# Optimization experiments

Measured on AMD Instinct MI355X. Metric: run time of the kernel, lower is better.

The kernel has to match this reference:

```python
import jax, jax.numpy as jnp
import numpy as np

NUM_HEADS = 16
Q_HEAD_DIM = 128
KV_HEAD_DIM = 128
ROPE_DIM = 64
LATENT_DIM = 512
INPUT_DIM = 2048


def setup_inputs() -> dict:
    key = jax.random.key(0)
    ks = jax.random.split(key, 7)
    B, S, D = 2, 2048, INPUT_DIM
    x = jax.random.normal(ks[0], (B, S, D), dtype=jnp.float32)
    positions = jnp.arange(S, dtype=jnp.int32)
    # weights stored as (in, out); torch Linear computes x @ W.T with W:(out,in)
    sc = lambda fan_in: 1.0 / np.sqrt(fan_in)
    Wq = jax.random.normal(ks[1], (D, NUM_HEADS * Q_HEAD_DIM), dtype=jnp.float32) * sc(D)
    Wc = jax.random.normal(ks[2], (D, LATENT_DIM), dtype=jnp.float32) * sc(D)
    Wk = jax.random.normal(ks[3], (LATENT_DIM, NUM_HEADS * KV_HEAD_DIM), dtype=jnp.float32) * sc(LATENT_DIM)
    Wv = jax.random.normal(ks[4], (LATENT_DIM, NUM_HEADS * KV_HEAD_DIM), dtype=jnp.float32) * sc(LATENT_DIM)
    Wo = jax.random.normal(ks[5], (NUM_HEADS * KV_HEAD_DIM, D), dtype=jnp.float32) * sc(NUM_HEADS * KV_HEAD_DIM)
    return {"x": x, "positions": positions, "Wq": Wq, "Wc": Wc, "Wk": Wk, "Wv": Wv, "Wo": Wo}


def _apply_rope_q(q, positions):
    # partial RoPE on first ROPE_DIM dims of q: (B,S,H,Dq)
    half = ROPE_DIM // 2
    inv_freq = 1.0 / (10000.0 ** (jnp.arange(0, ROPE_DIM, 2, dtype=jnp.float32) / ROPE_DIM))
    freqs = positions.astype(jnp.float32)[:, None] * inv_freq[None, :]  # (S, half)
    cos = jnp.cos(freqs)[None, :, None, :]  # (1,S,1,half)
    sin = jnp.sin(freqs)[None, :, None, :]
    x1 = q[..., :half]
    x2 = q[..., half:ROPE_DIM]
    rotated = jnp.concatenate([x1 * cos - x2 * sin, x1 * sin + x2 * cos], axis=-1)
    return jnp.concatenate([rotated, q[..., ROPE_DIM:]], axis=-1)


def reference(x, positions, Wq, Wc, Wk, Wv, Wo):
    B, S, _ = x.shape
    H, Dq, Dk = NUM_HEADS, Q_HEAD_DIM, KV_HEAD_DIM
    q = (x @ Wq).reshape(B, S, H, Dq)
    kv_latent = x @ Wc                       # (B,S,latent) low-rank compression
    k = (kv_latent @ Wk).reshape(B, S, H, Dk)
    v = (kv_latent @ Wv).reshape(B, S, H, Dk)
    q = _apply_rope_q(q, positions)          # RoPE applied to q only (as in source)
    scale = 1.0 / jnp.sqrt(jnp.float32(Dq))
    scores = jnp.einsum("bqhd,bkhd->bhqk", q, k) * scale
    attn = jax.nn.softmax(scores, axis=-1)
    out = jnp.einsum("bhqk,bkhd->bqhd", attn, v).reshape(B, S, H * Dk)
    return out @ Wo
```

## Files before the change

kernel.cpp:

```cpp
#include <hip/hip_runtime.h>
#include <math.h>


typedef __attribute__((ext_vector_type(8))) short bf16x8;
typedef __attribute__((ext_vector_type(4))) float f32x4;
typedef __attribute__((ext_vector_type(16))) float f32x16;

#define GLDS(gp, lp)                                                         \
  __builtin_amdgcn_global_load_lds(                                          \
      (const __attribute__((address_space(1))) void*)(gp),                   \
      (__attribute__((address_space(3))) void*)(lp), 16, 0, 0)

__device__ __forceinline__ short f2bf(float f) {
  unsigned u = __builtin_bit_cast(unsigned, f);
  u += 0x7fffu + ((u >> 16) & 1u);
  return (short)(u >> 16);
}
__device__ __forceinline__ float b2f(short x) {
  unsigned u = ((unsigned)(unsigned short)x) << 16;
  return __builtin_bit_cast(float, u);
}
__device__ __forceinline__ unsigned cvtpk(float lo, float hi) {
  unsigned r;
  asm("v_cvt_pk_bf16_f32 %0, %1, %2" : "=v"(r) : "v"(lo), "v"(hi));
  return r;
}

__global__ void cast4_kernel(const float* __restrict__ x, short* __restrict__ xb, int n4) {
  int i = blockIdx.x * blockDim.x + threadIdx.x;
  if (i < n4) {
    float4 v = ((const float4*)x)[i];
    ushort4 o;
    o.x = (unsigned short)f2bf(v.x);
    o.y = (unsigned short)f2bf(v.y);
    o.z = (unsigned short)f2bf(v.z);
    o.w = (unsigned short)f2bf(v.w);
    ((ushort4*)xb)[i] = o;
  }
}

__global__ void transpose_cast_kernel(const float* __restrict__ W, short* __restrict__ Wt,
                                      int K, int N) {
  __shared__ float tile[32][33];
  int n0 = blockIdx.x * 32, k0 = blockIdx.y * 32;
  int tx = threadIdx.x & 31, ty = threadIdx.x >> 5;
#pragma unroll
  for (int i = 0; i < 4; ++i)
    tile[ty + i * 8][tx] = W[(size_t)(k0 + ty + i * 8) * N + n0 + tx];
  __syncthreads();
#pragma unroll
  for (int i = 0; i < 4; ++i)
    Wt[(size_t)(n0 + ty + i * 8) * K + k0 + tx] = f2bf(tile[tx][ty + i * 8]);
}

__global__ void rope_tab_kernel(const int* __restrict__ pos, float* __restrict__ cosT,
                                float* __restrict__ sinT) {
  int idx = blockIdx.x * 256 + threadIdx.x;
  if (idx < 2048 * 32) {
    int s = idx >> 5, i = idx & 31;
    float p = (float)pos[s];
    float freq = p * powf(10000.0f, -(float)(2 * i) / 64.0f);
    float sv, cv;
    sincosf(freq, &sv, &cv);
    cosT[idx] = cv;
    sinT[idx] = sv;
  }
}

template <int MODE>
__global__ __launch_bounds__(256, 2) void gemm_bt(const short* __restrict__ A,
                                                  const short* __restrict__ Bt,
                                                  void* __restrict__ Cv,
                                                  int M, int N, int K) {
  __shared__ alignas(16) short sm[16384];
  const int tid  = threadIdx.x;
  const int lane = tid & 63;
  const int w    = tid >> 6;
  const int col  = lane & 15, g = lane >> 4;
  const int bm = blockIdx.y * 128, bn = blockIdx.x * 128;
  const int wr = w >> 1, wc = w & 1;

  f32x4 zero4 = {0.f, 0.f, 0.f, 0.f};
  f32x4 acc[4][4];
#pragma unroll
  for (int m = 0; m < 4; ++m)
#pragma unroll
    for (int n = 0; n < 4; ++n) acc[m][n] = zero4;

  const int srow = tid >> 2;
  const int skel = (tid & 3) * 8;
  const short* ag = A + (size_t)(bm + srow) * K + skel;
  const short* bg = Bt + (size_t)(bn + srow) * K + skel;

  auto STAGE = [&](int buf, int t) {
#pragma unroll
    for (int i = 0; i < 2; ++i) {
      GLDS(ag + (size_t)t * 32 + (size_t)i * 64 * K, sm + buf * 4096 + i * 2048 + w * 512);
      GLDS(bg + (size_t)t * 32 + (size_t)i * 64 * K, sm + 8192 + buf * 4096 + i * 2048 + w * 512);
    }
  };

  const int nt = K >> 5;
  STAGE(0, 0);
  __syncthreads();
  int buf = 0;
  for (int t = 0; t < nt; ++t) {
    if (t + 1 < nt) STAGE(buf ^ 1, t + 1);
    const short* As = sm + buf * 4096;
    const short* Bs = sm + 8192 + buf * 4096;
    bf16x8 la[4], lb[4];
#pragma unroll
    for (int m = 0; m < 4; ++m)
      la[m] = *(const bf16x8*)(As + (wr * 64 + m * 16 + col) * 32 + g * 8);
#pragma unroll
    for (int n = 0; n < 4; ++n)
      lb[n] = *(const bf16x8*)(Bs + (wc * 64 + n * 16 + col) * 32 + g * 8);
#pragma unroll
    for (int m = 0; m < 4; ++m)
#pragma unroll
      for (int n = 0; n < 4; ++n)
        acc[m][n] = __builtin_amdgcn_mfma_f32_16x16x32_bf16(la[m], lb[n], acc[m][n], 0, 0, 0);
    __syncthreads();
    buf ^= 1;
  }

  const int orow0 = bm + wr * 64;
  const int ocol0 = bn + wc * 64;
  if (MODE == 0) {
    short* C = (short*)Cv;
#pragma unroll
    for (int m = 0; m < 4; ++m)
#pragma unroll
      for (int n = 0; n < 4; ++n)
#pragma unroll
        for (int r = 0; r < 4; ++r)
          C[(size_t)(orow0 + m * 16 + g * 4 + r) * N + ocol0 + n * 16 + col] =
              f2bf(acc[m][n][r]);
  } else if (MODE == 1) {
    float* C = (float*)Cv;
#pragma unroll
    for (int m = 0; m < 4; ++m)
#pragma unroll
      for (int n = 0; n < 4; ++n)
#pragma unroll
        for (int r = 0; r < 4; ++r)
          C[(size_t)(orow0 + m * 16 + g * 4 + r) * N + ocol0 + n * 16 + col] =
              acc[m][n][r];
  } else {
    short* C = (short*)Cv;
#pragma unroll
    for (int m = 0; m < 4; ++m)
#pragma unroll
      for (int n = 0; n < 4; ++n) {
        int grow = orow0 + m * 16 + g * 4;
        int bb = grow >> 11, s = grow & 2047;
        int cn = ocol0 + n * 16 + col;
        ushort4 pk;
        pk.x = (unsigned short)f2bf(acc[m][n][0]);
        pk.y = (unsigned short)f2bf(acc[m][n][1]);
        pk.z = (unsigned short)f2bf(acc[m][n][2]);
        pk.w = (unsigned short)f2bf(acc[m][n][3]);
        *(ushort4*)(C + ((size_t)(bb * 2048 + cn)) * 2048 + s) = pk;
      }
  }
}

__global__ __launch_bounds__(256, 2) void attn_kernel(
    const short* __restrict__ qb, const short* __restrict__ kb,
    const short* __restrict__ vt, short* __restrict__ ob,
    const float* __restrict__ cosT, const float* __restrict__ sinT) {
  __shared__ alignas(16) short sm[32768];
  const int lane = threadIdx.x & 63, w = threadIdx.x >> 6;
  const int ql = lane & 31, hi = lane >> 5;
  const int qt = blockIdx.x >> 5, bh = blockIdx.x & 31;
  const int b = bh >> 4, h = bh & 15;
  const int q0w = qt * 128 + w * 32;
  const int qrow = q0w + ql;

  bf16x8 qf[8];
  {
    const short* qp = qb + ((size_t)(b * 2048 + qrow)) * 2048 + h * 128;
#pragma unroll
    for (int db = 0; db < 8; ++db) qf[db] = *(const bf16x8*)(qp + db * 16 + hi * 8);
    const float* cp = cosT + qrow * 32;
    const float* sp = sinT + qrow * 32;
#pragma unroll
    for (int db = 0; db < 2; ++db)
#pragma unroll
      for (int j = 0; j < 8; ++j) {
        int i = db * 16 + hi * 8 + j;
        float x1 = b2f(qf[db][j]), x2 = b2f(qf[db + 2][j]);
        float cv = cp[i], sv = sp[i];
        qf[db][j]     = f2bf(x1 * cv - x2 * sv);
        qf[db + 2][j] = f2bf(x1 * sv + x2 * cv);
      }
  }

  f32x16 o[4];
#pragma unroll
  for (int m4 = 0; m4 < 4; ++m4)
#pragma unroll
    for (int r = 0; r < 16; ++r) o[m4][r] = 0.f;
  float mrun = -3.0e38f, lrun = 0.f;

  auto STAGE = [&](int buf, int kt) {
#pragma unroll
    for (int i = 0; i < 4; ++i) {
      int r = w * 16 + i * 4 + (lane >> 4);
      int cch = lane & 15;
      const short* gp = kb + ((size_t)(b * 2048 + kt * 64 + r)) * 2048 + h * 128 +
                        ((cch ^ (r & 7)) << 3);
      GLDS(gp, sm + buf * 8192 + w * 2048 + i * 512);
    }
#pragma unroll
    for (int i = 0; i < 4; ++i) {
      int rd = w * 32 + i * 8 + (lane >> 3);
      int cch = lane & 7;
      const short* gp = vt + ((size_t)(b * 2048 + h * 128 + rd)) * 2048 + kt * 64 +
                        ((cch ^ (rd & 7)) << 3);
      GLDS(gp, sm + 16384 + buf * 8192 + w * 2048 + i * 512);
    }
  };

  const float cl2 = 0.12752744590518352f;
  STAGE(0, 0);
  __syncthreads();
  int buf = 0;
  for (int kt = 0; kt < 32; ++kt) {
    if (kt + 1 < 32) STAGE(buf ^ 1, kt + 1);
    const short* Ks = sm + buf * 8192;
    const short* Vs = sm + 16384 + buf * 8192;

    f32x16 skt[2];
    __builtin_amdgcn_s_setprio(1);
#pragma unroll
    for (int kb2 = 0; kb2 < 2; ++kb2) {
      f32x16 a;
#pragma unroll
      for (int r = 0; r < 16; ++r) a[r] = 0.f;
      int krow = kb2 * 32 + ql;
#pragma unroll
      for (int db = 0; db < 8; ++db) {
        bf16x8 kf = *(const bf16x8*)(Ks + krow * 128 + (((db * 2 + hi) ^ (krow & 7)) << 3));
        a = __builtin_amdgcn_mfma_f32_32x32x16_bf16(kf, qf[db], a, 0, 0, 0);
      }
      skt[kb2] = a;
    }
    __builtin_amdgcn_s_setprio(0);

#pragma unroll
    for (int kb2 = 0; kb2 < 2; ++kb2)
#pragma unroll
      for (int r = 0; r < 16; ++r) skt[kb2][r] *= cl2;

    float t0, t1, t2, t3;
    t0 = fmaxf(fmaxf(fmaxf(fmaxf(skt[0][0], skt[0][4]), skt[0][8]),
                     fmaxf(skt[0][12], skt[1][0])),
               fmaxf(fmaxf(skt[1][4], skt[1][8]), skt[1][12]));
    t1 = fmaxf(fmaxf(fmaxf(fmaxf(skt[0][1], skt[0][5]), skt[0][9]),
                     fmaxf(skt[0][13], skt[1][1])),
               fmaxf(fmaxf(skt[1][5], skt[1][9]), skt[1][13]));
    t2 = fmaxf(fmaxf(fmaxf(fmaxf(skt[0][2], skt[0][6]), skt[0][10]),
                     fmaxf(skt[0][14], skt[1][2])),
               fmaxf(fmaxf(skt[1][6], skt[1][10]), skt[1][14]));
    t3 = fmaxf(fmaxf(fmaxf(fmaxf(skt[0][3], skt[0][7]), skt[0][11]),
                     fmaxf(skt[0][15], skt[1][3])),
               fmaxf(fmaxf(skt[1][7], skt[1][11]), skt[1][15]));
    float tmax = fmaxf(fmaxf(t0, t1), fmaxf(t2, t3));
    tmax = fmaxf(tmax, __shfl_xor(tmax, 32));

    if (!__all(tmax <= mrun + 8.0f)) {
      float mn = fmaxf(mrun, tmax);
      float fr = __builtin_amdgcn_exp2f(mrun - mn);
      mrun = mn;
      lrun *= fr;
#pragma unroll
      for (int m4 = 0; m4 < 4; ++m4)
#pragma unroll
        for (int r = 0; r < 16; ++r) o[m4][r] *= fr;
    }
    float s0 = 0.f, s1 = 0.f, s2 = 0.f, s3 = 0.f;
#pragma unroll
    for (int kb2 = 0; kb2 < 2; ++kb2)
#pragma unroll
      for (int r = 0; r < 16; r += 4) {
        skt[kb2][r]     = __builtin_amdgcn_exp2f(skt[kb2][r] - mrun);
        skt[kb2][r + 1] = __builtin_amdgcn_exp2f(skt[kb2][r + 1] - mrun);
        skt[kb2][r + 2] = __builtin_amdgcn_exp2f(skt[kb2][r + 2] - mrun);
        skt[kb2][r + 3] = __builtin_amdgcn_exp2f(skt[kb2][r + 3] - mrun);
        s0 += skt[kb2][r];     s1 += skt[kb2][r + 1];
        s2 += skt[kb2][r + 2]; s3 += skt[kb2][r + 3];
      }
    float psum = (s0 + s1) + (s2 + s3);
    psum += __shfl_xor(psum, 32);
    lrun += psum;

    bf16x8 pf[4];
#pragma unroll
    for (int kb2 = 0; kb2 < 2; ++kb2) {
#pragma unroll
      for (int half = 0; half < 2; ++half) {
        unsigned a0 = cvtpk(skt[kb2][half * 8 + 0], skt[kb2][half * 8 + 1]);
        unsigned a1 = cvtpk(skt[kb2][half * 8 + 2], skt[kb2][half * 8 + 3]);
        unsigned b0 = cvtpk(skt[kb2][half * 8 + 4], skt[kb2][half * 8 + 5]);
        unsigned b1 = cvtpk(skt[kb2][half * 8 + 6], skt[kb2][half * 8 + 7]);
        unsigned pa0 = __shfl_xor(a0, 32), pa1 = __shfl_xor(a1, 32);
        unsigned pb0 = __shfl_xor(b0, 32), pb1 = __shfl_xor(b1, 32);
        union { unsigned u[4]; bf16x8 v; } tmp;
        tmp.u[0] = hi ? pb0 : a0;
        tmp.u[1] = hi ? pb1 : a1;
        tmp.u[2] = hi ? b0 : pa0;
        tmp.u[3] = hi ? b1 : pa1;
        pf[kb2 * 2 + half] = tmp.v;
      }
    }

    __builtin_amdgcn_s_setprio(1);
#pragma unroll
    for (int m4 = 0; m4 < 4; ++m4) {
      int rd = m4 * 32 + ql;
#pragma unroll
      for (int ks = 0; ks < 4; ++ks) {
        bf16x8 vf = *(const bf16x8*)(Vs + rd * 64 + (((ks * 2 + hi) ^ (rd & 7)) << 3));
        o[m4] = __builtin_amdgcn_mfma_f32_32x32x16_bf16(vf, pf[ks], o[m4], 0, 0, 0);
      }
    }
    __builtin_amdgcn_s_setprio(0);
    __syncthreads();
    buf ^= 1;
  }

  float il = 1.0f / lrun;
  short* E = sm + w * 4352;
#pragma unroll
  for (int m4 = 0; m4 < 4; ++m4)
#pragma unroll
    for (int r = 0; r < 16; r += 2) {
      int d = m4 * 32 + (r & 3) + 8 * (r >> 2) + 4 * hi;
      unsigned pk = cvtpk(o[m4][r] * il, o[m4][r + 1] * il);
      *(unsigned*)(E + ql * 136 + d) = pk;
    }
  asm volatile("s_waitcnt lgkmcnt(0)" ::: "memory");
#pragma unroll
  for (int it = 0; it < 8; ++it) {
    int row = it * 4 + (lane >> 4);
    int ch = lane & 15;
    bf16x8 v = *(const bf16x8*)(E + row * 136 + ch * 8);
    *(bf16x8*)(ob + ((size_t)(b * 2048 + q0w + row)) * 2048 + h * 128 + ch * 8) = v;
  }
}

extern "C" void kernel_launch(void* const* d_in, const int* in_sizes, int n_in,
                              void* d_out, int out_size, void* d_ws, size_t ws_size,
                              hipStream_t stream) {
  (void)in_sizes; (void)n_in; (void)out_size; (void)ws_size;
  const float* x  = (const float*)d_in[0];
  const int*   pos = (const int*)d_in[1];
  const float* Wq = (const float*)d_in[2];
  const float* Wc = (const float*)d_in[3];
  const float* Wk = (const float*)d_in[4];
  const float* Wv = (const float*)d_in[5];
  const float* Wo = (const float*)d_in[6];

  char* ws = (char*)d_ws;
  short* xb   = (short*)(ws);
  short* qb   = (short*)(ws + 16777216);
  short* kvb  = (short*)(ws + 33554432);
  short* kb   = (short*)(ws + 37748736);
  short* vtb  = (short*)(ws + 54525952);
  short* obuf = (short*)(ws + 71303168);
  short* wqT  = (short*)(ws + 88080384);
  short* wcT  = (short*)(ws + 96468992);
  short* wkT  = (short*)(ws + 98566144);
  short* wvT  = (short*)(ws + 100663296);
  short* woT  = (short*)(ws + 102760448);
  float* cosT = (float*)(ws + 111149056);
  float* sinT = (float*)(ws + 111411200);

  cast4_kernel<<<8192, 256, 0, stream>>>(x, xb, 2097152);
  transpose_cast_kernel<<<dim3(64, 64), 256, 0, stream>>>(Wq, wqT, 2048, 2048);
  transpose_cast_kernel<<<dim3(16, 64), 256, 0, stream>>>(Wc, wcT, 2048, 512);
  transpose_cast_kernel<<<dim3(64, 16), 256, 0, stream>>>(Wk, wkT, 512, 2048);
  transpose_cast_kernel<<<dim3(64, 16), 256, 0, stream>>>(Wv, wvT, 512, 2048);
  transpose_cast_kernel<<<dim3(64, 64), 256, 0, stream>>>(Wo, woT, 2048, 2048);
  rope_tab_kernel<<<256, 256, 0, stream>>>(pos, cosT, sinT);

  gemm_bt<0><<<dim3(16, 32), 256, 0, stream>>>(xb, wqT, qb, 4096, 2048, 2048);
  gemm_bt<0><<<dim3(4, 32), 256, 0, stream>>>(xb, wcT, kvb, 4096, 512, 2048);
  gemm_bt<0><<<dim3(16, 32), 256, 0, stream>>>(kvb, wkT, kb, 4096, 2048, 512);
  gemm_bt<2><<<dim3(16, 32), 256, 0, stream>>>(kvb, wvT, vtb, 4096, 2048, 512);

  attn_kernel<<<512, 256, 0, stream>>>(qb, kb, vtb, obuf, cosT, sinT);

  gemm_bt<1><<<dim3(16, 32), 256, 0, stream>>>(obuf, woT, (float*)d_out, 4096, 2048, 2048);
}
```

Baseline: 272.0 us.

## Deepen GEMM K-tile to 64 with XOR-swizzled LDS and merge GEMM launches

The GEMM core now stages 64-wide K tiles instead of 32, and uses an XOR swizzle on the LDS column index to avoid bank conflicts on fragment reads. It halves the number of barrier-separated iterations. Independent GEMMs (Q with compression, K with V) and the weight transpose-casts are merged into fewer launches so they fill the GPU together and cut launch overhead. The cost is doubled LDS per block (64KB), which may reduce occupancy below the requested 2 blocks per CU.

```diff
diff --git a/kernel.cpp b/kernel.cpp
--- a/kernel.cpp
+++ b/kernel.cpp
@@ -39,8 +39,11 @@
   }
 }
 
-__global__ void transpose_cast_kernel(const float* __restrict__ W, short* __restrict__ Wt,
-                                      int K, int N) {
+__global__ void transpose_cast2_kernel(const float* __restrict__ W0, short* __restrict__ T0,
+                                       const float* __restrict__ W1, short* __restrict__ T1,
+                                       int K, int N) {
+  const float* W = blockIdx.z ? W1 : W0;
+  short* Wt = blockIdx.z ? T1 : T0;
   __shared__ float tile[32][33];
   int n0 = blockIdx.x * 32, k0 = blockIdx.y * 32;
   int tx = threadIdx.x & 31, ty = threadIdx.x >> 5;
@@ -68,16 +71,15 @@
 }
 
 template <int MODE>
-__global__ __launch_bounds__(256, 2) void gemm_bt(const short* __restrict__ A,
-                                                  const short* __restrict__ Bt,
-                                                  void* __restrict__ Cv,
-                                                  int M, int N, int K) {
-  __shared__ alignas(16) short sm[16384];
+__device__ __forceinline__ void gemm_core(const short* __restrict__ A,
+                                          const short* __restrict__ Bt,
+                                          void* __restrict__ Cv,
+                                          int N, int K, int bm, int bn,
+                                          short* sm) {
   const int tid  = threadIdx.x;
   const int lane = tid & 63;
   const int w    = tid >> 6;
   const int col  = lane & 15, g = lane >> 4;
-  const int bm = blockIdx.y * 128, bn = blockIdx.x * 128;
   const int wr = w >> 1, wc = w & 1;
 
   f32x4 zero4 = {0.f, 0.f, 0.f, 0.f};
@@ -87,39 +89,48 @@
 #pragma unroll
     for (int n = 0; n < 4; ++n) acc[m][n] = zero4;
 
-  const int srow = tid >> 2;
-  const int skel = (tid & 3) * 8;
-  const short* ag = A + (size_t)(bm + srow) * K + skel;
-  const short* bg = Bt + (size_t)(bn + srow) * K + skel;
+  const int sr = tid >> 3;
+  const int sk = tid & 7;
 
   auto STAGE = [&](int buf, int t) {
 #pragma unroll
-    for (int i = 0; i < 2; ++i) {
-      GLDS(ag + (size_t)t * 32 + (size_t)i * 64 * K, sm + buf * 4096 + i * 2048 + w * 512);
-      GLDS(bg + (size_t)t * 32 + (size_t)i * 64 * K, sm + 8192 + buf * 4096 + i * 2048 + w * 512);
+    for (int i = 0; i < 4; ++i) {
+      int r = i * 32 + sr;
+      int c = (sk ^ (r & 7)) << 3;
+      GLDS(A  + (size_t)(bm + r) * K + t * 64 + c,
+           sm + buf * 8192 + i * 2048 + w * 512);
+      GLDS(Bt + (size_t)(bn + r) * K + t * 64 + c,
+           sm + 16384 + buf * 8192 + i * 2048 + w * 512);
     }
   };
 
-  const int nt = K >> 5;
+  const int nt = K >> 6;
   STAGE(0, 0);
   __syncthreads();
   int buf = 0;
   for (int t = 0; t < nt; ++t) {
     if (t + 1 < nt) STAGE(buf ^ 1, t + 1);
-    const short* As = sm + buf * 4096;
-    const short* Bs = sm + 8192 + buf * 4096;
-    bf16x8 la[4], lb[4];
-#pragma unroll
-    for (int m = 0; m < 4; ++m)
-      la[m] = *(const bf16x8*)(As + (wr * 64 + m * 16 + col) * 32 + g * 8);
-#pragma unroll
-    for (int n = 0; n < 4; ++n)
-      lb[n] = *(const bf16x8*)(Bs + (wc * 64 + n * 16 + col) * 32 + g * 8);
-#pragma unroll
-    for (int m = 0; m < 4; ++m)
-#pragma unroll
-      for (int n = 0; n < 4; ++n)
-        acc[m][n] = __builtin_amdgcn_mfma_f32_16x16x32_bf16(la[m], lb[n], acc[m][n], 0, 0, 0);
+    const short* As = sm + buf * 8192;
+    const short* Bs = sm + 16384 + buf * 8192;
+#pragma unroll
+    for (int kk = 0; kk < 2; ++kk) {
+      bf16x8 la[4], lb[4];
+#pragma unroll
+      for (int m = 0; m < 4; ++m) {
+        int row = wr * 64 + m * 16 + col;
+        la[m] = *(const bf16x8*)(As + row * 64 + (((kk * 4 + g) ^ (row & 7)) << 3));
+      }
+#pragma unroll
+      for (int n = 0; n < 4; ++n) {
+        int row = wc * 64 + n * 16 + col;
+        lb[n] = *(const bf16x8*)(Bs + row * 64 + (((kk * 4 + g) ^ (row & 7)) << 3));
+      }
+#pragma unroll
+      for (int m = 0; m < 4; ++m)
+#pragma unroll
+        for (int n = 0; n < 4; ++n)
+          acc[m][n] = __builtin_amdgcn_mfma_f32_16x16x32_bf16(la[m], lb[n], acc[m][n], 0, 0, 0);
+    }
     __syncthreads();
     buf ^= 1;
   }
@@ -163,6 +174,33 @@
         *(ushort4*)(C + ((size_t)(bb * 2048 + cn)) * 2048 + s) = pk;
       }
   }
+}
+
+__global__ __launch_bounds__(256, 2) void gemm_qc(const short* __restrict__ xb,
+                                                  const short* __restrict__ wqT,
+                                                  const short* __restrict__ wcT,
+                                                  short* __restrict__ qb,
+                                                  short* __restrict__ kvb) {
+  __shared__ alignas(16) short sm[32768];
+  int x = blockIdx.x, y = blockIdx.y;
+  if (x < 16) gemm_core<0>(xb, wqT, qb, 2048, 2048, y * 128, x * 128, sm);
+  else        gemm_core<0>(xb, wcT, kvb, 512, 2048, y * 128, (x - 16) * 128, sm);
+}
+__global__ __launch_bounds__(256, 2) void gemm_kv(const short* __restrict__ kvb,
+                                                  const short* __restrict__ wkT,
+                                                  const short* __restrict__ wvT,
+                                                  short* __restrict__ kb,
+                                                  short* __restrict__ vtb) {
+  __shared__ alignas(16) short sm[32768];
+  int x = blockIdx.x, y = blockIdx.y;
+  if (x < 16) gemm_core<0>(kvb, wkT, kb, 2048, 512, y * 128, x * 128, sm);
+  else        gemm_core<2>(kvb, wvT, vtb, 2048, 512, y * 128, (x - 16) * 128, sm);
+}
+__global__ __launch_bounds__(256, 2) void gemm_wo(const short* __restrict__ obuf,
+                                                  const short* __restrict__ woT,
+                                                  float* __restrict__ out) {
+  __shared__ alignas(16) short sm[32768];
+  gemm_core<1>(obuf, woT, out, 2048, 2048, blockIdx.y * 128, blockIdx.x * 128, sm);
 }
 
 __global__ __launch_bounds__(256, 2) void attn_kernel(
@@ -378,19 +416,15 @@
   float* sinT = (float*)(ws + 111411200);
 
   cast4_kernel<<<8192, 256, 0, stream>>>(x, xb, 2097152);
-  transpose_cast_kernel<<<dim3(64, 64), 256, 0, stream>>>(Wq, wqT, 2048, 2048);
-  transpose_cast_kernel<<<dim3(16, 64), 256, 0, stream>>>(Wc, wcT, 2048, 512);
-  transpose_cast_kernel<<<dim3(64, 16), 256, 0, stream>>>(Wk, wkT, 512, 2048);
-  transpose_cast_kernel<<<dim3(64, 16), 256, 0, stream>>>(Wv, wvT, 512, 2048);
-  transpose_cast_kernel<<<dim3(64, 64), 256, 0, stream>>>(Wo, woT, 2048, 2048);
+  transpose_cast2_kernel<<<dim3(64, 64, 2), 256, 0, stream>>>(Wq, wqT, Wo, woT, 2048, 2048);
+  transpose_cast2_kernel<<<dim3(16, 64, 1), 256, 0, stream>>>(Wc, wcT, Wc, wcT, 2048, 512);
+  transpose_cast2_kernel<<<dim3(64, 16, 2), 256, 0, stream>>>(Wk, wkT, Wv, wvT, 512, 2048);
   rope_tab_kernel<<<256, 256, 0, stream>>>(pos, cosT, sinT);
 
-  gemm_bt<0><<<dim3(16, 32), 256, 0, stream>>>(xb, wqT, qb, 4096, 2048, 2048);
-  gemm_bt<0><<<dim3(4, 32), 256, 0, stream>>>(xb, wcT, kvb, 4096, 512, 2048);
-  gemm_bt<0><<<dim3(16, 32), 256, 0, stream>>>(kvb, wkT, kb, 4096, 2048, 512);
-  gemm_bt<2><<<dim3(16, 32), 256, 0, stream>>>(kvb, wvT, vtb, 4096, 2048, 512);
+  gemm_qc<<<dim3(20, 32), 256, 0, stream>>>(xb, wqT, wcT, qb, kvb);
+  gemm_kv<<<dim3(32, 32), 256, 0, stream>>>(kvb, wkT, wvT, kb, vtb);
 
   attn_kernel<<<512, 256, 0, stream>>>(qb, kb, vtb, obuf, cosT, sinT);
 
-  gemm_bt<1><<<dim3(16, 32), 256, 0, stream>>>(obuf, woT, (float*)d_out, 4096, 2048, 2048);
-}
+  gemm_wo<<<dim3(16, 32), 256, 0, stream>>>(obuf, woT, (float*)d_out);
+}
```

New measurement: 232.0 us. -14.7%, faster.
